# Performance work log

Measured on AMD Instinct MI355X. Metric: run time of the kernel, lower is better.

## Reference

```python
import jax, jax.numpy as jnp
import numpy as np
from jax import lax

BS, K, N = 8, 8, 16            # batch, gathers per sample, picks per curve
T, WG = 3072, 64               # gather time samples, traces
H, WC = 256, 256               # CVEncoder ScaleSize
RH, RW = 1024, 512             # resize (also GatherEncoder outLen=RH)
T0, T1 = 0.0, 7000.0           # tInt[0], tInt[-1]


def setup_inputs() -> dict:
    key = jax.random.key(0)
    ks = jax.random.split(key, 8)
    gather = jax.random.normal(ks[0], (BS, K, T, WG), jnp.float32)
    # cv: times sorted, strictly > 0, within [T0, T1]; velocities within VMM range
    times = jnp.sort(jax.random.uniform(ks[1], (BS, K, N), minval=100.0, maxval=T1), axis=-1)
    vels = jnp.sort(jax.random.uniform(ks[2], (BS, K, N), minval=1500.0, maxval=4500.0), axis=-1)
    cv = jnp.stack([times, vels], axis=-1).astype(jnp.float32)
    VMM = jnp.tile(jnp.array([1500.0, 4500.0], jnp.float32), (BS, 1))
    def cw(k, shape):
        return (jax.random.normal(k, shape, jnp.float32) * 0.1)
    params = dict(
        w1=cw(ks[3], (1, 1, 3, 3)), b1=jnp.zeros((1,), jnp.float32), g1=jnp.ones((1,), jnp.float32), be1=jnp.zeros((1,), jnp.float32),
        w2=cw(ks[4], (2, 3, 3, 3)), b2=jnp.zeros((2,), jnp.float32), g2=jnp.ones((2,), jnp.float32), be2=jnp.zeros((2,), jnp.float32),
        w3=cw(ks[5], (1, 2, 3, 2)), b3=jnp.zeros((1,), jnp.float32), g3=jnp.ones((1,), jnp.float32), be3=jnp.zeros((1,), jnp.float32),
        wf=cw(ks[6], (1, 1, 3, 3)), bf=jnp.zeros((1,), jnp.float32), gf=jnp.ones((1,), jnp.float32), bef=jnp.zeros((1,), jnp.float32),
    )
    return {"gather": gather, "cv": cv, "VMM": VMM, **params}


def _conv(x, w, b, stride, pad):
    y = lax.conv_general_dilated(x, w, stride, pad, dimension_numbers=("NCHW", "OIHW", "NCHW"))
    return y + b[None, :, None, None]


def _bn(x, g, b, eps=1e-5):
    # training-mode BatchNorm2d: stats over (N, H, W)
    m = jnp.mean(x, (0, 2, 3), keepdims=True)
    v = jnp.var(x, (0, 2, 3), keepdims=True)
    return (x - m) / jnp.sqrt(v + eps) * g[None, :, None, None] + b[None, :, None, None]


def _lrelu(x):
    return jnp.where(x >= 0, x, 0.1 * x)


def _cbl(x, w, b, g, be, stride):
    return _lrelu(_bn(_conv(x, w, b, stride, "VALID"), g, be))


def _maxpool(x, k):
    p = k // 2
    return lax.reduce_window(x, -jnp.inf, lax.max, (1, 1, k, k), (1, 1, 1, 1),
                             ((0, 0), (0, 0), (p, p), (p, p)))


def _cv_mask(cv, VMM):
    # normalize times to fractional row index and velocities to fractional col index
    dt = (T1 - T0) / (H - 1)
    t_idx = (cv[..., 0] - T0) / dt                                        # (BS,K,N)
    dv = (VMM[:, 1] - VMM[:, 0]) / (WC - 1)                               # (BS,)
    v_idx = (cv[..., 1] - VMM[:, 0, None, None]) / dv[:, None, None]      # (BS,K,N)
    t_flat = t_idx.reshape(-1, N)
    v_flat = v_idx.reshape(-1, N)
    tq = jnp.arange(H, dtype=jnp.float32)
    # per-curve piecewise-linear interpolation of v over the time grid
    v_curve = jax.vmap(lambda xp, fp: jnp.interp(tq, xp, fp))(t_flat, v_flat)  # (M,H)
    v_int = jnp.clip(v_curve.astype(jnp.int32), 0, WC - 1)
    M = BS * K
    mask = jnp.full((M, H, WC), 0.01, jnp.float32)
    mask = mask.at[jnp.arange(M)[:, None], jnp.arange(H)[None, :], v_int].add(0.9)
    mask = mask.reshape(BS, K, H, WC)
    # bilinear resize, half-pixel centers == torch align_corners=False
    return jax.image.resize(mask, (BS, K, RH, RW), method="linear")


def _forward(gather, cv, VMM, w1, b1, g1, be1, w2, b2, g2, be2, w3, b3, g3, be3, wf, bf, gf, bef):
    cv_mask = lax.stop_gradient(_cv_mask(cv, VMM))          # CVEncoder runs under no_grad
    x = gather.reshape(-1, 1, T, WG)                        # (BS*K,1,T,WG)
    x = x / jnp.max(jnp.abs(x))                             # mode='mute': keep sign
    x = _cbl(x, w1, b1, g1, be1, (3, 2))                    # (M,1,1024,31)
    xcat = jnp.concatenate([x, _maxpool(x, 3), _maxpool(x, 5)], axis=1)
    x = _cbl(xcat, w2, b2, g2, be2, (3, 2))                 # (M,2,341,15)
    x = _cbl(x, w3, b3, g3, be3, (3, 2))                    # (M,1,113,7)
    x = jax.image.resize(x, (x.shape[0], 1, RH, 1), method="linear")
    genr = x.reshape(BS, K, RH, 1)
    mix = jnp.sum(genr * cv_mask, axis=1, keepdims=True)    # (BS,1,RH,RW)
    y = _conv(mix, wf, bf, (1, 1), ((1, 1), (1, 1)))
    return _lrelu(_bn(y, gf, bef))


def reference(gather, cv, VMM, w1, b1, g1, be1, w2, b2, g2, be2, w3, b3, g3, be3, wf, bf, gf, bef):
    return _forward(gather, cv, VMM, w1, b1, g1, be1, w2, b2, g2, be2, w3, b3, g3, be3, wf, bf, gf, bef)
```

## Files before the change

kernel.cpp:

```cpp
#include <hip/hip_runtime.h>
#include <math.h>

#define BSZ 8
#define KG  8
#define NP  16
#define MM  64
#define TT  3072
#define WGN 64
#define HH  256
#define WCN 256
#define RHN 1024
#define RWN 512

#define C1H 1024
#define C1W 31
#define C2H 341
#define C2W 15
#define C3H 113
#define C3W 7

#define N1 (MM*C1H*C1W)
#define N2 (MM*C2H*C2W)
#define N3 (MM*C3H*C3W)
#define NF (BSZ*RHN*RWN)

#define SL 8

#define OFF_VINT 768
#define OFF_Y1   (OFF_VINT + MM*HH*4)
#define OFF_Y2   (OFF_Y1  + N1*4)
#define OFF_Y3   (OFF_Y2  + 2*N2*4)
#define OFF_GENR (OFF_Y3  + N3*4)

__device__ __forceinline__ void blockAdd2(double s, double ss, double* o0, double* o1) {
    __shared__ double red[4][2];
    __syncthreads();
    int lane = threadIdx.x & 63, wid = threadIdx.x >> 6;
#pragma unroll
    for (int off = 32; off > 0; off >>= 1) {
        s  += __shfl_down(s,  off, 64);
        ss += __shfl_down(ss, off, 64);
    }
    if (lane == 0) { red[wid][0] = s; red[wid][1] = ss; }
    __syncthreads();
    if (threadIdx.x == 0) {
        double a = 0, b = 0;
        int nw = blockDim.x >> 6;
        for (int i = 0; i < nw; i++) { a += red[i][0]; b += red[i][1]; }
        int slot = blockIdx.x & (SL - 1);
        atomicAdd(&o0[slot], a); atomicAdd(&o1[slot], b);
    }
}

__device__ __forceinline__ float2 bn_ab(const double* __restrict__ sums, int c,
                                        const float* __restrict__ g,
                                        const float* __restrict__ be, double n) {
    double sum = 0, sumsq = 0;
#pragma unroll
    for (int j = 0; j < SL; j++) {
        sum   += sums[(2 * c) * SL + j];
        sumsq += sums[(2 * c + 1) * SL + j];
    }
    double mean = sum / n;
    double var  = sumsq / n - mean * mean;
    double a = (double)g[c] / sqrt(var + 1e-5);
    return make_float2((float)a, (float)((double)be[c] - mean * a));
}

__global__ void k_conv1(const float* __restrict__ g, const float* __restrict__ w1,
                        const float* __restrict__ b1,
                        float* __restrict__ y1, double* sums) {
    float w[9];
#pragma unroll
    for (int i = 0; i < 9; i++) w[i] = w1[i];
    float bb = b1[0];
    double s = 0, ss = 0;
    int stride = gridDim.x * blockDim.x;
    for (int idx = blockIdx.x * blockDim.x + threadIdx.x; idx < N1; idx += stride) {
        int ow = idx % C1W;
        int t2 = idx / C1W;
        int oh = t2 % C1H;
        int m  = t2 / C1H;
        const float* xp = g + (size_t)m * TT * WGN + (size_t)(oh * 3) * WGN + ow * 2;
        float acc = bb;
#pragma unroll
        for (int r = 0; r < 3; r++)
#pragma unroll
            for (int c = 0; c < 3; c++) acc += w[r * 3 + c] * xp[r * WGN + c];
        y1[idx] = acc;
        s += acc; ss += (double)acc * (double)acc;
    }
    blockAdd2(s, ss, &sums[0], &sums[SL]);
}

#define F2_OH 32
#define F2_NCH 11
#define F2_NRMAX (3*F2_OH + 4)
__global__ void k_fused2(const float* __restrict__ y1, const double* __restrict__ sums_r,
                         const float* __restrict__ g1, const float* __restrict__ be1,
                         const float* __restrict__ w2, const float* __restrict__ b2,
                         float* __restrict__ y2, double* sums) {
    __shared__ float sact[F2_NRMAX][32];
    __shared__ float sr3[F2_NRMAX][32];
    __shared__ float sr5[F2_NRMAX][32];
    float2 ab1 = bn_ab(sums_r, 0, g1, be1, (double)N1);
    int m   = blockIdx.x / F2_NCH;
    int ch  = blockIdx.x % F2_NCH;
    int oh0 = ch * F2_OH;
    int OHa = min(F2_OH, C2H - oh0);
    int NR  = 3 * OHa + 4;
    int gl0 = 3 * oh0 - 2;
    const float* yp = y1 + (size_t)m * C1H * C1W;
    for (int i = threadIdx.x; i < NR * C1W; i += blockDim.x) {
        int l = i / C1W, w = i % C1W;
        int gr = gl0 + l;
        float v = -INFINITY;
        if (gr >= 0 && gr < C1H) {
            v = ab1.x * yp[gr * C1W + w] + ab1.y;
            v = v >= 0.f ? v : 0.1f * v;
        }
        sact[l][w] = v;
    }
    __syncthreads();
    for (int i = threadIdx.x; i < NR * C1W; i += blockDim.x) {
        int l = i / C1W, w = i % C1W;
        int wl1 = max(w - 1, 0), wr1 = min(w + 1, C1W - 1);
        int wl2 = max(w - 2, 0), wr2 = min(w + 2, C1W - 1);
        float c  = sact[l][w];
        float m3 = fmaxf(fmaxf(sact[l][wl1], c), sact[l][wr1]);
        float m5 = fmaxf(fmaxf(m3, sact[l][wl2]), sact[l][wr2]);
        sr3[l][w] = m3;
        sr5[l][w] = m5;
    }
    __syncthreads();
    double s0 = 0, ss0 = 0, s1 = 0, ss1 = 0;
    for (int o = threadIdx.x; o < OHa * C2W; o += blockDim.x) {
        int lo = o / C2W, ow = o % C2W;
        float a0 = b2[0], acc1 = b2[1];
#pragma unroll
        for (int i = 0; i < 3; i++) {
            int l = 3 * lo + 2 + i;
#pragma unroll
            for (int j = 0; j < 3; j++) {
                int wc = 2 * ow + j;
                float v0 = sact[l][wc];
                float v1 = fmaxf(fmaxf(sr3[l - 1][wc], sr3[l][wc]), sr3[l + 1][wc]);
                float v2 = fmaxf(fmaxf(fmaxf(sr5[l - 2][wc], sr5[l - 1][wc]), sr5[l][wc]),
                                 fmaxf(sr5[l + 1][wc], sr5[l + 2][wc]));
                int ki = i * 3 + j;
                a0   += w2[ki] * v0 + w2[9 + ki] * v1 + w2[18 + ki] * v2;
                acc1 += w2[27 + ki] * v0 + w2[36 + ki] * v1 + w2[45 + ki] * v2;
            }
        }
        size_t ob = (size_t)m * (2 * C2H * C2W) + (size_t)(oh0 + lo) * C2W + ow;
        y2[ob] = a0;
        y2[ob + C2H * C2W] = acc1;
        s0 += a0; ss0 += (double)a0 * a0;
        s1 += acc1; ss1 += (double)acc1 * acc1;
    }
    blockAdd2(s0, ss0, &sums[2 * SL], &sums[3 * SL]);
    blockAdd2(s1, ss1, &sums[4 * SL], &sums[5 * SL]);
}

__global__ void k_conv3(const float* __restrict__ y2, const double* __restrict__ sums_r,
                        const float* __restrict__ g2, const float* __restrict__ be2,
                        const float* __restrict__ w3, const float* __restrict__ b3,
                        float* __restrict__ y3, double* sums) {
    float2 ab20 = bn_ab(sums_r + 2 * SL, 0, g2, be2, (double)N2);
    float2 ab21 = bn_ab(sums_r + 2 * SL, 1, g2, be2, (double)N2);
    double s = 0, ss = 0;
    int stride = gridDim.x * blockDim.x;
    for (int idx = blockIdx.x * blockDim.x + threadIdx.x; idx < N3; idx += stride) {
        int ow = idx % C3W;
        int t2 = idx / C3W;
        int oh = t2 % C3H;
        int m  = t2 / C3H;
        float acc = b3[0];
#pragma unroll
        for (int i = 0; i < 2; i++) {
            float aa = i ? ab21.x : ab20.x, bb = i ? ab21.y : ab20.y;
            const float* cp = y2 + (size_t)m * (2 * C2H * C2W) + (size_t)i * C2H * C2W
                              + (size_t)(oh * 3) * C2W + ow * 2;
#pragma unroll
            for (int r = 0; r < 3; r++)
#pragma unroll
                for (int c = 0; c < 2; c++) {
                    float v = aa * cp[r * C2W + c] + bb;
                    v = v >= 0.f ? v : 0.1f * v;
                    acc += w3[i * 6 + r * 2 + c] * v;
                }
        }
        y3[idx] = acc;
        s += acc; ss += (double)acc * acc;
    }
    blockAdd2(s, ss, &sums[6 * SL], &sums[7 * SL]);
}

__global__ void k_vintgenr(const float* __restrict__ cv, const float* __restrict__ VMM,
                           const float* __restrict__ y3, const double* __restrict__ sums_r,
                           const float* __restrict__ g3, const float* __restrict__ be3,
                           int* __restrict__ vint, float* __restrict__ genr) {
    __shared__ float tt[NP], vv[NP];
    __shared__ float tile[C3H * C3W];
    int m = blockIdx.x;
    int b = m >> 3;
    float2 ab3 = bn_ab(sums_r + 6 * SL, 0, g3, be3, (double)N3);
    if (threadIdx.x < NP) {
        int n = threadIdx.x;
        float t = cv[(m * NP + n) * 2 + 0];
        float v = cv[(m * NP + n) * 2 + 1];
        float dt = 7000.0f / 255.0f;
        tt[n] = t / dt;
        float vmin = VMM[b * 2], vmax = VMM[b * 2 + 1];
        float dv = (vmax - vmin) / 255.0f;
        vv[n] = (v - vmin) / dv;
    }
    for (int i = threadIdx.x; i < C3H * C3W; i += blockDim.x) {
        float v = ab3.x * y3[m * C3H * C3W + i] + ab3.y;
        tile[i] = v >= 0.f ? v : 0.1f * v;
    }
    __syncthreads();
    {
        int h = threadIdx.x;
        float x = (float)h;
        float val;
        if (x <= tt[0]) val = vv[0];
        else if (x >= tt[NP - 1]) val = vv[NP - 1];
        else {
            int i = 1;
            while (i < NP - 1 && tt[i] <= x) i++;
            float d = tt[i] - tt[i - 1];
            val = (d != 0.f) ? vv[i - 1] + (x - tt[i - 1]) / d * (vv[i] - vv[i - 1]) : vv[i];
        }
        int vi = (int)val;
        vint[m * HH + h] = max(0, min(WCN - 1, vi));
    }
    const float cw0 = 4.f / 37.f, cw1 = 5.f / 37.f, cw2 = 6.f / 37.f, cw3 = 7.f / 37.f;
    const float cw[7] = { cw0, cw1, cw2, cw3, cw2, cw1, cw0 };
    for (int i = threadIdx.x; i < RHN; i += blockDim.x) {
        float sh = (i + 0.5f) * (113.0f / 1024.0f) - 0.5f;
        float fl = floorf(sh);
        float fr = sh - fl;
        int i0 = (int)fl, i1 = i0 + 1;
        i0 = max(0, min(C3H - 1, i0));
        i1 = max(0, min(C3H - 1, i1));
        float acc = 0.f;
#pragma unroll
        for (int x = 0; x < 7; x++) {
            float v = (1.f - fr) * tile[i0 * C3W + x] + fr * tile[i1 * C3W + x];
            acc += cw[x] * v;
        }
        genr[m * RHN + i] = acc;
    }
}

#define MC_TH 16
__device__ __forceinline__ void build_mix_tile(const float* __restrict__ genr,
                                               const int* __restrict__ vint,
                                               int b, int h0,
                                               float (*tile)[RWN + 2], float* Grow) {
    for (int i = threadIdx.x; i < (MC_TH + 2) * (RWN + 2); i += blockDim.x)
        ((float*)tile)[i] = 0.f;
    if (threadIdx.x < MC_TH + 2) Grow[threadIdx.x] = 0.f;
    __syncthreads();
    if (threadIdx.x < (MC_TH + 2) * KG) {
        int r = threadIdx.x / KG, k = threadIdx.x % KG;
        int h = h0 - 1 + r;
        if (h >= 0 && h < RHN) {
            int m = b * KG + k;
            float g = genr[m * RHN + h];
            atomicAdd(&Grow[r], g);
            float sh = (h + 0.5f) * 0.25f - 0.5f;
            float fl = floorf(sh);
            float fh = sh - fl;
            int ih0 = (int)fl, ih1 = ih0 + 1;
            ih0 = max(0, min(HH - 1, ih0));
            ih1 = max(0, min(HH - 1, ih1));
            int vv[2] = { vint[m * HH + ih0], vint[m * HH + ih1] };
            float aa[2] = { 0.9f * g * (1.f - fh), 0.9f * g * fh };
#pragma unroll
            for (int t = 0; t < 2; t++) {
                int v = vv[t]; float A = aa[t];
                if (v == 0) {
                    atomicAdd(&tile[r][1 + 0], A);
                    atomicAdd(&tile[r][1 + 1], 0.75f * A);
                    atomicAdd(&tile[r][1 + 2], 0.25f * A);
                } else if (v == WCN - 1) {
                    atomicAdd(&tile[r][1 + 509], 0.25f * A);
                    atomicAdd(&tile[r][1 + 510], 0.75f * A);
                    atomicAdd(&tile[r][1 + 511], A);
                } else {
                    atomicAdd(&tile[r][1 + 2 * v - 1], 0.25f * A);
                    atomicAdd(&tile[r][1 + 2 * v],     0.75f * A);
                    atomicAdd(&tile[r][1 + 2 * v + 1], 0.75f * A);
                    atomicAdd(&tile[r][1 + 2 * v + 2], 0.25f * A);
                }
            }
        }
    }
    __syncthreads();
    for (int i = threadIdx.x; i < (MC_TH + 2) * RWN; i += blockDim.x) {
        int r = i / RWN, w = i % RWN;
        int h = h0 - 1 + r;
        if (h >= 0 && h < RHN) tile[r][w + 1] += 0.01f * Grow[r];
    }
    __syncthreads();
}

__global__ void k_mixA(const float* __restrict__ genr, const int* __restrict__ vint,
                       const float* __restrict__ wf, const float* __restrict__ bf,
                       double* sums) {
    __shared__ float tile[MC_TH + 2][RWN + 2];
    __shared__ float Grow[MC_TH + 2];
    int b   = blockIdx.x / (RHN / MC_TH);
    int h0  = (blockIdx.x % (RHN / MC_TH)) * MC_TH;
    build_mix_tile(genr, vint, b, h0, tile, Grow);
    float w[9];
#pragma unroll
    for (int i = 0; i < 9; i++) w[i] = wf[i];
    float bb = bf[0];
    double s = 0, ss = 0;
    for (int o = threadIdx.x; o < MC_TH * RWN; o += blockDim.x) {
        int lr = o / RWN, x = o % RWN;
        float acc = bb;
#pragma unroll
        for (int dr = 0; dr < 3; dr++)
#pragma unroll
            for (int dc = 0; dc < 3; dc++)
                acc += w[dr * 3 + dc] * tile[lr + dr][x + dc];
        s += acc; ss += (double)acc * acc;
    }
    blockAdd2(s, ss, &sums[8 * SL], &sums[9 * SL]);
}

__global__ void k_mixB(const float* __restrict__ genr, const int* __restrict__ vint,
                       const float* __restrict__ wf, const float* __restrict__ bf,
                       const double* __restrict__ sums_r, const float* __restrict__ gf,
                       const float* __restrict__ bef, float* __restrict__ out) {
    __shared__ float tile[MC_TH + 2][RWN + 2];
    __shared__ float Grow[MC_TH + 2];
    float2 abf = bn_ab(sums_r + 8 * SL, 0, gf, bef, (double)NF);
    int b   = blockIdx.x / (RHN / MC_TH);
    int h0  = (blockIdx.x % (RHN / MC_TH)) * MC_TH;
    build_mix_tile(genr, vint, b, h0, tile, Grow);
    float w[9];
#pragma unroll
    for (int i = 0; i < 9; i++) w[i] = wf[i];
    float bb = bf[0];
    for (int o = threadIdx.x; o < MC_TH * RWN; o += blockDim.x) {
        int lr = o / RWN, x = o % RWN;
        float acc = bb;
#pragma unroll
        for (int dr = 0; dr < 3; dr++)
#pragma unroll
            for (int dc = 0; dc < 3; dc++)
                acc += w[dr * 3 + dc] * tile[lr + dr][x + dc];
        float v = abf.x * acc + abf.y;
        out[((size_t)b * RHN + (h0 + lr)) * RWN + x] = v >= 0.f ? v : 0.1f * v;
    }
}

extern "C" void kernel_launch(void* const* d_in, const int* in_sizes, int n_in,
                              void* d_out, int out_size, void* d_ws, size_t ws_size,
                              hipStream_t stream) {
    const float* gather = (const float*)d_in[0];
    const float* cv     = (const float*)d_in[1];
    const float* VMM    = (const float*)d_in[2];
    const float* w1 = (const float*)d_in[3];
    const float* b1 = (const float*)d_in[4];
    const float* g1 = (const float*)d_in[5];
    const float* be1 = (const float*)d_in[6];
    const float* w2 = (const float*)d_in[7];
    const float* b2 = (const float*)d_in[8];
    const float* g2 = (const float*)d_in[9];
    const float* be2 = (const float*)d_in[10];
    const float* w3 = (const float*)d_in[11];
    const float* b3 = (const float*)d_in[12];
    const float* g3 = (const float*)d_in[13];
    const float* be3 = (const float*)d_in[14];
    const float* wf = (const float*)d_in[15];
    const float* bf = (const float*)d_in[16];
    const float* gf = (const float*)d_in[17];
    const float* bef = (const float*)d_in[18];
    float* out = (float*)d_out;

    char* ws = (char*)d_ws;
    double* sums = (double*)ws;
    int*   vint  = (int*)(ws + OFF_VINT);
    float* y1    = (float*)(ws + OFF_Y1);
    float* y2    = (float*)(ws + OFF_Y2);
    float* y3    = (float*)(ws + OFF_Y3);
    float* genr  = (float*)(ws + OFF_GENR);

    hipMemsetAsync(d_ws, 0, 640, stream);

    k_conv1<<<512, 256, 0, stream>>>(gather, w1, b1, y1, sums);
    k_fused2<<<MM * F2_NCH, 256, 0, stream>>>(y1, sums, g1, be1, w2, b2, y2, sums);
    k_conv3<<<198, 256, 0, stream>>>(y2, sums, g2, be2, w3, b3, y3, sums);
    k_vintgenr<<<MM, 256, 0, stream>>>(cv, VMM, y3, sums, g3, be3, vint, genr);
    k_mixA<<<BSZ * (RHN / MC_TH), 256, 0, stream>>>(genr, vint, wf, bf, sums);
    k_mixB<<<BSZ * (RHN / MC_TH), 256, 0, stream>>>(genr, vint, wf, bf, sums, gf, bef, out);
}
```

Before: 196.9 us.

## Fuse all stages into one cooperative persistent kernel with grid syncs

Replaces six separate kernel launches with a single cooperative kernel of 512 blocks that uses grid.sync between the BatchNorm-dependent stages. The final mix conv keeps its 32 outputs per thread in registers, so the tile is built and convolved once instead of being rebuilt in a second pass just to apply BN. Conv1 now stages gather tiles in shared memory with float4 loads. This removes launch gaps and the duplicated mix work, at the cost of grid-wide barriers, a fixed grid size and register pressure from the accumulator array.

```diff
diff --git a/kernel.cpp b/kernel.cpp
--- a/kernel.cpp
+++ b/kernel.cpp
@@ -1,5 +1,8 @@
 #include <hip/hip_runtime.h>
+#include <hip/hip_cooperative_groups.h>
 #include <math.h>
+
+namespace cg = cooperative_groups;
 
 #define BSZ 8
 #define KG  8
@@ -25,6 +28,8 @@
 #define NF (BSZ*RHN*RWN)
 
 #define SL 8
+#define GRID 512
+#define BLK  256
 
 #define OFF_VINT 768
 #define OFF_Y1   (OFF_VINT + MM*HH*4)
@@ -32,7 +37,11 @@
 #define OFF_Y3   (OFF_Y2  + 2*N2*4)
 #define OFF_GENR (OFF_Y3  + N3*4)
 
-__device__ __forceinline__ void blockAdd2(double s, double ss, double* o0, double* o1) {
+#define MC_TH 16
+#define SMEM_BYTES 38400
+
+__device__ __forceinline__ void blockAdd2(double s, double ss, double* o0, double* o1,
+                                          int slot) {
     __shared__ double red[4][2];
     __syncthreads();
     int lane = threadIdx.x & 63, wid = threadIdx.x >> 6;
@@ -45,9 +54,8 @@
     __syncthreads();
     if (threadIdx.x == 0) {
         double a = 0, b = 0;
-        int nw = blockDim.x >> 6;
-        for (int i = 0; i < nw; i++) { a += red[i][0]; b += red[i][1]; }
-        int slot = blockIdx.x & (SL - 1);
+#pragma unroll
+        for (int i = 0; i < 4; i++) { a += red[i][0]; b += red[i][1]; }
         atomicAdd(&o0[slot], a); atomicAdd(&o1[slot], b);
     }
 }
@@ -67,296 +75,304 @@
     return make_float2((float)a, (float)((double)be[c] - mean * a));
 }
 
-__global__ void k_conv1(const float* __restrict__ g, const float* __restrict__ w1,
-                        const float* __restrict__ b1,
-                        float* __restrict__ y1, double* sums) {
-    float w[9];
-#pragma unroll
-    for (int i = 0; i < 9; i++) w[i] = w1[i];
-    float bb = b1[0];
-    double s = 0, ss = 0;
-    int stride = gridDim.x * blockDim.x;
-    for (int idx = blockIdx.x * blockDim.x + threadIdx.x; idx < N1; idx += stride) {
-        int ow = idx % C1W;
-        int t2 = idx / C1W;
-        int oh = t2 % C1H;
-        int m  = t2 / C1H;
-        const float* xp = g + (size_t)m * TT * WGN + (size_t)(oh * 3) * WGN + ow * 2;
-        float acc = bb;
-#pragma unroll
-        for (int r = 0; r < 3; r++)
-#pragma unroll
-            for (int c = 0; c < 3; c++) acc += w[r * 3 + c] * xp[r * WGN + c];
-        y1[idx] = acc;
-        s += acc; ss += (double)acc * (double)acc;
-    }
-    blockAdd2(s, ss, &sums[0], &sums[SL]);
-}
-
 #define F2_OH 32
 #define F2_NCH 11
-#define F2_NRMAX (3*F2_OH + 4)
-__global__ void k_fused2(const float* __restrict__ y1, const double* __restrict__ sums_r,
-                         const float* __restrict__ g1, const float* __restrict__ be1,
-                         const float* __restrict__ w2, const float* __restrict__ b2,
-                         float* __restrict__ y2, double* sums) {
-    __shared__ float sact[F2_NRMAX][32];
-    __shared__ float sr3[F2_NRMAX][32];
-    __shared__ float sr5[F2_NRMAX][32];
-    float2 ab1 = bn_ab(sums_r, 0, g1, be1, (double)N1);
-    int m   = blockIdx.x / F2_NCH;
-    int ch  = blockIdx.x % F2_NCH;
-    int oh0 = ch * F2_OH;
-    int OHa = min(F2_OH, C2H - oh0);
-    int NR  = 3 * OHa + 4;
-    int gl0 = 3 * oh0 - 2;
-    const float* yp = y1 + (size_t)m * C1H * C1W;
-    for (int i = threadIdx.x; i < NR * C1W; i += blockDim.x) {
-        int l = i / C1W, w = i % C1W;
-        int gr = gl0 + l;
-        float v = -INFINITY;
-        if (gr >= 0 && gr < C1H) {
-            v = ab1.x * yp[gr * C1W + w] + ab1.y;
-            v = v >= 0.f ? v : 0.1f * v;
-        }
-        sact[l][w] = v;
-    }
-    __syncthreads();
-    for (int i = threadIdx.x; i < NR * C1W; i += blockDim.x) {
-        int l = i / C1W, w = i % C1W;
-        int wl1 = max(w - 1, 0), wr1 = min(w + 1, C1W - 1);
-        int wl2 = max(w - 2, 0), wr2 = min(w + 2, C1W - 1);
-        float c  = sact[l][w];
-        float m3 = fmaxf(fmaxf(sact[l][wl1], c), sact[l][wr1]);
-        float m5 = fmaxf(fmaxf(m3, sact[l][wl2]), sact[l][wr2]);
-        sr3[l][w] = m3;
-        sr5[l][w] = m5;
-    }
-    __syncthreads();
-    double s0 = 0, ss0 = 0, s1 = 0, ss1 = 0;
-    for (int o = threadIdx.x; o < OHa * C2W; o += blockDim.x) {
-        int lo = o / C2W, ow = o % C2W;
-        float a0 = b2[0], acc1 = b2[1];
-#pragma unroll
-        for (int i = 0; i < 3; i++) {
-            int l = 3 * lo + 2 + i;
-#pragma unroll
-            for (int j = 0; j < 3; j++) {
-                int wc = 2 * ow + j;
-                float v0 = sact[l][wc];
-                float v1 = fmaxf(fmaxf(sr3[l - 1][wc], sr3[l][wc]), sr3[l + 1][wc]);
-                float v2 = fmaxf(fmaxf(fmaxf(sr5[l - 2][wc], sr5[l - 1][wc]), sr5[l][wc]),
-                                 fmaxf(sr5[l + 1][wc], sr5[l + 2][wc]));
-                int ki = i * 3 + j;
-                a0   += w2[ki] * v0 + w2[9 + ki] * v1 + w2[18 + ki] * v2;
-                acc1 += w2[27 + ki] * v0 + w2[36 + ki] * v1 + w2[45 + ki] * v2;
-            }
-        }
-        size_t ob = (size_t)m * (2 * C2H * C2W) + (size_t)(oh0 + lo) * C2W + ow;
-        y2[ob] = a0;
-        y2[ob + C2H * C2W] = acc1;
-        s0 += a0; ss0 += (double)a0 * a0;
-        s1 += acc1; ss1 += (double)acc1 * acc1;
-    }
-    blockAdd2(s0, ss0, &sums[2 * SL], &sums[3 * SL]);
-    blockAdd2(s1, ss1, &sums[4 * SL], &sums[5 * SL]);
-}
-
-__global__ void k_conv3(const float* __restrict__ y2, const double* __restrict__ sums_r,
-                        const float* __restrict__ g2, const float* __restrict__ be2,
-                        const float* __restrict__ w3, const float* __restrict__ b3,
-                        float* __restrict__ y3, double* sums) {
-    float2 ab20 = bn_ab(sums_r + 2 * SL, 0, g2, be2, (double)N2);
-    float2 ab21 = bn_ab(sums_r + 2 * SL, 1, g2, be2, (double)N2);
-    double s = 0, ss = 0;
-    int stride = gridDim.x * blockDim.x;
-    for (int idx = blockIdx.x * blockDim.x + threadIdx.x; idx < N3; idx += stride) {
-        int ow = idx % C3W;
-        int t2 = idx / C3W;
-        int oh = t2 % C3H;
-        int m  = t2 / C3H;
-        float acc = b3[0];
-#pragma unroll
-        for (int i = 0; i < 2; i++) {
-            float aa = i ? ab21.x : ab20.x, bb = i ? ab21.y : ab20.y;
-            const float* cp = y2 + (size_t)m * (2 * C2H * C2W) + (size_t)i * C2H * C2W
-                              + (size_t)(oh * 3) * C2W + ow * 2;
-#pragma unroll
-            for (int r = 0; r < 3; r++)
-#pragma unroll
-                for (int c = 0; c < 2; c++) {
-                    float v = aa * cp[r * C2W + c] + bb;
+
+__global__ void __launch_bounds__(BLK, 2) k_mega(
+        const float* __restrict__ gather, const float* __restrict__ cv,
+        const float* __restrict__ VMM,
+        const float* __restrict__ w1, const float* __restrict__ b1,
+        const float* __restrict__ g1, const float* __restrict__ be1,
+        const float* __restrict__ w2, const float* __restrict__ b2,
+        const float* __restrict__ g2, const float* __restrict__ be2,
+        const float* __restrict__ w3, const float* __restrict__ b3,
+        const float* __restrict__ g3, const float* __restrict__ be3,
+        const float* __restrict__ wf, const float* __restrict__ bf,
+        const float* __restrict__ gf, const float* __restrict__ bef,
+        double* sums, int* vint, float* y1, float* y2, float* y3, float* genr,
+        float* out) {
+    cg::grid_group grid = cg::this_grid();
+    __shared__ __align__(16) char smem[SMEM_BYTES];
+    int slot = blockIdx.x & (SL - 1);
+
+    {
+        float (*S1)[WGN] = (float (*)[WGN])smem;
+        float w[9];
+#pragma unroll
+        for (int i = 0; i < 9; i++) w[i] = w1[i];
+        float bb = b1[0];
+        double s = 0, ss = 0;
+        for (int tile = blockIdx.x; tile < MM * 32; tile += GRID) {
+            int m = tile >> 5, t32 = tile & 31;
+            int oh0 = t32 * F2_OH;
+            const float4* g4 = (const float4*)(gather + (size_t)m * TT * WGN
+                                               + (size_t)(3 * oh0) * WGN);
+            float4* s4 = (float4*)smem;
+            __syncthreads();
+#pragma unroll
+            for (int i = threadIdx.x; i < 96 * WGN / 4; i += BLK) s4[i] = g4[i];
+            __syncthreads();
+#pragma unroll
+            for (int j = 0; j < 4; j++) {
+                int o = threadIdx.x + j * BLK;
+                if (o < F2_OH * C1W) {
+                    int lo = o / C1W, ow = o % C1W;
+                    float acc = bb;
+#pragma unroll
+                    for (int r = 0; r < 3; r++)
+#pragma unroll
+                        for (int c = 0; c < 3; c++)
+                            acc += w[r * 3 + c] * S1[3 * lo + r][2 * ow + c];
+                    y1[(size_t)m * C1H * C1W + (size_t)(oh0 + lo) * C1W + ow] = acc;
+                    s += acc; ss += (double)acc * acc;
+                }
+            }
+        }
+        blockAdd2(s, ss, &sums[0], &sums[SL], slot);
+    }
+    __threadfence(); grid.sync();
+
+    {
+        float (*sact)[32] = (float (*)[32])smem;
+        float (*sr3)[32]  = (float (*)[32])(smem + 12800);
+        float (*sr5)[32]  = (float (*)[32])(smem + 25600);
+        float2 ab1 = bn_ab(sums, 0, g1, be1, (double)N1);
+        double s0 = 0, ss0 = 0, s1 = 0, ss1 = 0;
+        for (int vb = blockIdx.x; vb < MM * F2_NCH; vb += GRID) {
+            int m   = vb / F2_NCH;
+            int ch  = vb % F2_NCH;
+            int oh0 = ch * F2_OH;
+            int OHa = min(F2_OH, C2H - oh0);
+            int NR  = 3 * OHa + 4;
+            int gl0 = 3 * oh0 - 2;
+            const float* yp = y1 + (size_t)m * C1H * C1W;
+            __syncthreads();
+            for (int i = threadIdx.x; i < NR * C1W; i += BLK) {
+                int l = i / C1W, w = i % C1W;
+                int gr = gl0 + l;
+                float v = -INFINITY;
+                if (gr >= 0 && gr < C1H) {
+                    v = ab1.x * yp[gr * C1W + w] + ab1.y;
                     v = v >= 0.f ? v : 0.1f * v;
-                    acc += w3[i * 6 + r * 2 + c] * v;
                 }
-        }
-        y3[idx] = acc;
-        s += acc; ss += (double)acc * acc;
-    }
-    blockAdd2(s, ss, &sums[6 * SL], &sums[7 * SL]);
-}
-
-__global__ void k_vintgenr(const float* __restrict__ cv, const float* __restrict__ VMM,
-                           const float* __restrict__ y3, const double* __restrict__ sums_r,
-                           const float* __restrict__ g3, const float* __restrict__ be3,
-                           int* __restrict__ vint, float* __restrict__ genr) {
-    __shared__ float tt[NP], vv[NP];
-    __shared__ float tile[C3H * C3W];
-    int m = blockIdx.x;
-    int b = m >> 3;
-    float2 ab3 = bn_ab(sums_r + 6 * SL, 0, g3, be3, (double)N3);
-    if (threadIdx.x < NP) {
-        int n = threadIdx.x;
-        float t = cv[(m * NP + n) * 2 + 0];
-        float v = cv[(m * NP + n) * 2 + 1];
-        float dt = 7000.0f / 255.0f;
-        tt[n] = t / dt;
-        float vmin = VMM[b * 2], vmax = VMM[b * 2 + 1];
-        float dv = (vmax - vmin) / 255.0f;
-        vv[n] = (v - vmin) / dv;
-    }
-    for (int i = threadIdx.x; i < C3H * C3W; i += blockDim.x) {
-        float v = ab3.x * y3[m * C3H * C3W + i] + ab3.y;
-        tile[i] = v >= 0.f ? v : 0.1f * v;
-    }
-    __syncthreads();
+                sact[l][w] = v;
+            }
+            __syncthreads();
+            for (int i = threadIdx.x; i < NR * C1W; i += BLK) {
+                int l = i / C1W, w = i % C1W;
+                int wl1 = max(w - 1, 0), wr1 = min(w + 1, C1W - 1);
+                int wl2 = max(w - 2, 0), wr2 = min(w + 2, C1W - 1);
+                float c  = sact[l][w];
+                float m3 = fmaxf(fmaxf(sact[l][wl1], c), sact[l][wr1]);
+                float m5 = fmaxf(fmaxf(m3, sact[l][wl2]), sact[l][wr2]);
+                sr3[l][w] = m3;
+                sr5[l][w] = m5;
+            }
+            __syncthreads();
+            for (int o = threadIdx.x; o < OHa * C2W; o += BLK) {
+                int lo = o / C2W, ow = o % C2W;
+                float a0 = b2[0], acc1 = b2[1];
+#pragma unroll
+                for (int i = 0; i < 3; i++) {
+                    int l = 3 * lo + 2 + i;
+#pragma unroll
+                    for (int j = 0; j < 3; j++) {
+                        int wc = 2 * ow + j;
+                        float v0 = sact[l][wc];
+                        float v1 = fmaxf(fmaxf(sr3[l - 1][wc], sr3[l][wc]), sr3[l + 1][wc]);
+                        float v2 = fmaxf(fmaxf(fmaxf(sr5[l - 2][wc], sr5[l - 1][wc]),
+                                               sr5[l][wc]),
+                                         fmaxf(sr5[l + 1][wc], sr5[l + 2][wc]));
+                        int ki = i * 3 + j;
+                        a0   += w2[ki] * v0 + w2[9 + ki] * v1 + w2[18 + ki] * v2;
+                        acc1 += w2[27 + ki] * v0 + w2[36 + ki] * v1 + w2[45 + ki] * v2;
+                    }
+                }
+                size_t ob = (size_t)m * (2 * C2H * C2W) + (size_t)(oh0 + lo) * C2W + ow;
+                y2[ob] = a0;
+                y2[ob + C2H * C2W] = acc1;
+                s0 += a0; ss0 += (double)a0 * a0;
+                s1 += acc1; ss1 += (double)acc1 * acc1;
+            }
+        }
+        blockAdd2(s0, ss0, &sums[2 * SL], &sums[3 * SL], slot);
+        blockAdd2(s1, ss1, &sums[4 * SL], &sums[5 * SL], slot);
+    }
+    __threadfence(); grid.sync();
+
     {
-        int h = threadIdx.x;
-        float x = (float)h;
-        float val;
-        if (x <= tt[0]) val = vv[0];
-        else if (x >= tt[NP - 1]) val = vv[NP - 1];
-        else {
-            int i = 1;
-            while (i < NP - 1 && tt[i] <= x) i++;
-            float d = tt[i] - tt[i - 1];
-            val = (d != 0.f) ? vv[i - 1] + (x - tt[i - 1]) / d * (vv[i] - vv[i - 1]) : vv[i];
-        }
-        int vi = (int)val;
-        vint[m * HH + h] = max(0, min(WCN - 1, vi));
-    }
-    const float cw0 = 4.f / 37.f, cw1 = 5.f / 37.f, cw2 = 6.f / 37.f, cw3 = 7.f / 37.f;
-    const float cw[7] = { cw0, cw1, cw2, cw3, cw2, cw1, cw0 };
-    for (int i = threadIdx.x; i < RHN; i += blockDim.x) {
-        float sh = (i + 0.5f) * (113.0f / 1024.0f) - 0.5f;
-        float fl = floorf(sh);
-        float fr = sh - fl;
-        int i0 = (int)fl, i1 = i0 + 1;
-        i0 = max(0, min(C3H - 1, i0));
-        i1 = max(0, min(C3H - 1, i1));
-        float acc = 0.f;
-#pragma unroll
-        for (int x = 0; x < 7; x++) {
-            float v = (1.f - fr) * tile[i0 * C3W + x] + fr * tile[i1 * C3W + x];
-            acc += cw[x] * v;
-        }
-        genr[m * RHN + i] = acc;
-    }
-}
-
-#define MC_TH 16
-__device__ __forceinline__ void build_mix_tile(const float* __restrict__ genr,
-                                               const int* __restrict__ vint,
-                                               int b, int h0,
-                                               float (*tile)[RWN + 2], float* Grow) {
-    for (int i = threadIdx.x; i < (MC_TH + 2) * (RWN + 2); i += blockDim.x)
-        ((float*)tile)[i] = 0.f;
-    if (threadIdx.x < MC_TH + 2) Grow[threadIdx.x] = 0.f;
-    __syncthreads();
-    if (threadIdx.x < (MC_TH + 2) * KG) {
-        int r = threadIdx.x / KG, k = threadIdx.x % KG;
-        int h = h0 - 1 + r;
-        if (h >= 0 && h < RHN) {
-            int m = b * KG + k;
-            float g = genr[m * RHN + h];
-            atomicAdd(&Grow[r], g);
-            float sh = (h + 0.5f) * 0.25f - 0.5f;
+        float2 ab20 = bn_ab(sums + 2 * SL, 0, g2, be2, (double)N2);
+        float2 ab21 = bn_ab(sums + 2 * SL, 1, g2, be2, (double)N2);
+        double s = 0, ss = 0;
+        for (int idx = blockIdx.x * BLK + threadIdx.x; idx < N3; idx += GRID * BLK) {
+            int ow = idx % C3W;
+            int t2 = idx / C3W;
+            int oh = t2 % C3H;
+            int m  = t2 / C3H;
+            float acc = b3[0];
+#pragma unroll
+            for (int i = 0; i < 2; i++) {
+                float aa = i ? ab21.x : ab20.x, bb = i ? ab21.y : ab20.y;
+                const float* cp = y2 + (size_t)m * (2 * C2H * C2W) + (size_t)i * C2H * C2W
+                                  + (size_t)(oh * 3) * C2W + ow * 2;
+#pragma unroll
+                for (int r = 0; r < 3; r++)
+#pragma unroll
+                    for (int c = 0; c < 2; c++) {
+                        float v = aa * cp[r * C2W + c] + bb;
+                        v = v >= 0.f ? v : 0.1f * v;
+                        acc += w3[i * 6 + r * 2 + c] * v;
+                    }
+            }
+            y3[idx] = acc;
+            s += acc; ss += (double)acc * acc;
+        }
+        blockAdd2(s, ss, &sums[6 * SL], &sums[7 * SL], slot);
+    }
+    __threadfence(); grid.sync();
+
+    if (blockIdx.x < MM) {
+        float* tts  = (float*)smem;
+        float* vvs  = tts + NP;
+        float* tile = vvs + NP;
+        int m = blockIdx.x;
+        int b = m >> 3;
+        float2 ab3 = bn_ab(sums + 6 * SL, 0, g3, be3, (double)N3);
+        __syncthreads();
+        if (threadIdx.x < NP) {
+            int n = threadIdx.x;
+            float t = cv[(m * NP + n) * 2 + 0];
+            float v = cv[(m * NP + n) * 2 + 1];
+            float dt = 7000.0f / 255.0f;
+            tts[n] = t / dt;
+            float vmin = VMM[b * 2], vmax = VMM[b * 2 + 1];
+            float dv = (vmax - vmin) / 255.0f;
+            vvs[n] = (v - vmin) / dv;
+        }
+        for (int i = threadIdx.x; i < C3H * C3W; i += BLK) {
+            float v = ab3.x * y3[m * C3H * C3W + i] + ab3.y;
+            tile[i] = v >= 0.f ? v : 0.1f * v;
+        }
+        __syncthreads();
+        {
+            int h = threadIdx.x;
+            float x = (float)h;
+            float val;
+            if (x <= tts[0]) val = vvs[0];
+            else if (x >= tts[NP - 1]) val = vvs[NP - 1];
+            else {
+                int i = 1;
+                while (i < NP - 1 && tts[i] <= x) i++;
+                float d = tts[i] - tts[i - 1];
+                val = (d != 0.f) ? vvs[i - 1] + (x - tts[i - 1]) / d * (vvs[i] - vvs[i - 1])
+                                 : vvs[i];
+            }
+            int vi = (int)val;
+            vint[m * HH + h] = max(0, min(WCN - 1, vi));
+        }
+        const float cwv[7] = { 4.f/37.f, 5.f/37.f, 6.f/37.f, 7.f/37.f,
+                               6.f/37.f, 5.f/37.f, 4.f/37.f };
+        for (int i = threadIdx.x; i < RHN; i += BLK) {
+            float sh = (i + 0.5f) * (113.0f / 1024.0f) - 0.5f;
             float fl = floorf(sh);
-            float fh = sh - fl;
-            int ih0 = (int)fl, ih1 = ih0 + 1;
-            ih0 = max(0, min(HH - 1, ih0));
-            ih1 = max(0, min(HH - 1, ih1));
-            int vv[2] = { vint[m * HH + ih0], vint[m * HH + ih1] };
-            float aa[2] = { 0.9f * g * (1.f - fh), 0.9f * g * fh };
-#pragma unroll
-            for (int t = 0; t < 2; t++) {
-                int v = vv[t]; float A = aa[t];
-                if (v == 0) {
-                    atomicAdd(&tile[r][1 + 0], A);
-                    atomicAdd(&tile[r][1 + 1], 0.75f * A);
-                    atomicAdd(&tile[r][1 + 2], 0.25f * A);
-                } else if (v == WCN - 1) {
-                    atomicAdd(&tile[r][1 + 509], 0.25f * A);
-                    atomicAdd(&tile[r][1 + 510], 0.75f * A);
-                    atomicAdd(&tile[r][1 + 511], A);
-                } else {
-                    atomicAdd(&tile[r][1 + 2 * v - 1], 0.25f * A);
-                    atomicAdd(&tile[r][1 + 2 * v],     0.75f * A);
-                    atomicAdd(&tile[r][1 + 2 * v + 1], 0.75f * A);
-                    atomicAdd(&tile[r][1 + 2 * v + 2], 0.25f * A);
+            float fr = sh - fl;
+            int i0 = (int)fl, i1 = i0 + 1;
+            i0 = max(0, min(C3H - 1, i0));
+            i1 = max(0, min(C3H - 1, i1));
+            float acc = 0.f;
+#pragma unroll
+            for (int x = 0; x < 7; x++) {
+                float v = (1.f - fr) * tile[i0 * C3W + x] + fr * tile[i1 * C3W + x];
+                acc += cwv[x] * v;
+            }
+            genr[m * RHN + i] = acc;
+        }
+    }
+    __threadfence(); grid.sync();
+
+    float accv[32];
+    int b5  = blockIdx.x >> 6;
+    int h0  = (blockIdx.x & 63) * MC_TH;
+    {
+        float (*tile)[RWN + 2] = (float (*)[RWN + 2])smem;
+        float* Grow = (float*)(smem + (MC_TH + 2) * (RWN + 2) * 4);
+        for (int i = threadIdx.x; i < (MC_TH + 2) * (RWN + 2); i += BLK)
+            ((float*)tile)[i] = 0.f;
+        if (threadIdx.x < MC_TH + 2) Grow[threadIdx.x] = 0.f;
+        __syncthreads();
+        if (threadIdx.x < (MC_TH + 2) * KG) {
+            int r = threadIdx.x / KG, k = threadIdx.x % KG;
+            int h = h0 - 1 + r;
+            if (h >= 0 && h < RHN) {
+                int m = b5 * KG + k;
+                float g = genr[m * RHN + h];
+                atomicAdd(&Grow[r], g);
+                float sh = (h + 0.5f) * 0.25f - 0.5f;
+                float fl = floorf(sh);
+                float fh = sh - fl;
+                int ih0 = (int)fl, ih1 = ih0 + 1;
+                ih0 = max(0, min(HH - 1, ih0));
+                ih1 = max(0, min(HH - 1, ih1));
+                int vv2[2] = { vint[m * HH + ih0], vint[m * HH + ih1] };
+                float aa2[2] = { 0.9f * g * (1.f - fh), 0.9f * g * fh };
+#pragma unroll
+                for (int t = 0; t < 2; t++) {
+                    int v = vv2[t]; float A = aa2[t];
+                    if (v == 0) {
+                        atomicAdd(&tile[r][1 + 0], A);
+                        atomicAdd(&tile[r][1 + 1], 0.75f * A);
+                        atomicAdd(&tile[r][1 + 2], 0.25f * A);
+                    } else if (v == WCN - 1) {
+                        atomicAdd(&tile[r][1 + 509], 0.25f * A);
+                        atomicAdd(&tile[r][1 + 510], 0.75f * A);
+                        atomicAdd(&tile[r][1 + 511], A);
+                    } else {
+                        atomicAdd(&tile[r][1 + 2 * v - 1], 0.25f * A);
+                        atomicAdd(&tile[r][1 + 2 * v],     0.75f * A);
+                        atomicAdd(&tile[r][1 + 2 * v + 1], 0.75f * A);
+                        atomicAdd(&tile[r][1 + 2 * v + 2], 0.25f * A);
+                    }
                 }
             }
         }
-    }
-    __syncthreads();
-    for (int i = threadIdx.x; i < (MC_TH + 2) * RWN; i += blockDim.x) {
-        int r = i / RWN, w = i % RWN;
-        int h = h0 - 1 + r;
-        if (h >= 0 && h < RHN) tile[r][w + 1] += 0.01f * Grow[r];
-    }
-    __syncthreads();
-}
-
-__global__ void k_mixA(const float* __restrict__ genr, const int* __restrict__ vint,
-                       const float* __restrict__ wf, const float* __restrict__ bf,
-                       double* sums) {
-    __shared__ float tile[MC_TH + 2][RWN + 2];
-    __shared__ float Grow[MC_TH + 2];
-    int b   = blockIdx.x / (RHN / MC_TH);
-    int h0  = (blockIdx.x % (RHN / MC_TH)) * MC_TH;
-    build_mix_tile(genr, vint, b, h0, tile, Grow);
-    float w[9];
-#pragma unroll
-    for (int i = 0; i < 9; i++) w[i] = wf[i];
-    float bb = bf[0];
-    double s = 0, ss = 0;
-    for (int o = threadIdx.x; o < MC_TH * RWN; o += blockDim.x) {
-        int lr = o / RWN, x = o % RWN;
-        float acc = bb;
-#pragma unroll
-        for (int dr = 0; dr < 3; dr++)
-#pragma unroll
-            for (int dc = 0; dc < 3; dc++)
-                acc += w[dr * 3 + dc] * tile[lr + dr][x + dc];
-        s += acc; ss += (double)acc * acc;
-    }
-    blockAdd2(s, ss, &sums[8 * SL], &sums[9 * SL]);
-}
-
-__global__ void k_mixB(const float* __restrict__ genr, const int* __restrict__ vint,
-                       const float* __restrict__ wf, const float* __restrict__ bf,
-                       const double* __restrict__ sums_r, const float* __restrict__ gf,
-                       const float* __restrict__ bef, float* __restrict__ out) {
-    __shared__ float tile[MC_TH + 2][RWN + 2];
-    __shared__ float Grow[MC_TH + 2];
-    float2 abf = bn_ab(sums_r + 8 * SL, 0, gf, bef, (double)NF);
-    int b   = blockIdx.x / (RHN / MC_TH);
-    int h0  = (blockIdx.x % (RHN / MC_TH)) * MC_TH;
-    build_mix_tile(genr, vint, b, h0, tile, Grow);
-    float w[9];
-#pragma unroll
-    for (int i = 0; i < 9; i++) w[i] = wf[i];
-    float bb = bf[0];
-    for (int o = threadIdx.x; o < MC_TH * RWN; o += blockDim.x) {
-        int lr = o / RWN, x = o % RWN;
-        float acc = bb;
-#pragma unroll
-        for (int dr = 0; dr < 3; dr++)
-#pragma unroll
-            for (int dc = 0; dc < 3; dc++)
-                acc += w[dr * 3 + dc] * tile[lr + dr][x + dc];
-        float v = abf.x * acc + abf.y;
-        out[((size_t)b * RHN + (h0 + lr)) * RWN + x] = v >= 0.f ? v : 0.1f * v;
+        __syncthreads();
+        for (int i = threadIdx.x; i < (MC_TH + 2) * RWN; i += BLK) {
+            int r = i / RWN, w = i % RWN;
+            int h = h0 - 1 + r;
+            if (h >= 0 && h < RHN) tile[r][w + 1] += 0.01f * Grow[r];
+        }
+        __syncthreads();
+        float w[9];
+#pragma unroll
+        for (int i = 0; i < 9; i++) w[i] = wf[i];
+        float bb = bf[0];
+        double s = 0, ss = 0;
+#pragma unroll
+        for (int j = 0; j < 32; j++) {
+            int o  = threadIdx.x + j * BLK;
+            int lr = o >> 9, x = o & 511;
+            float acc = bb;
+#pragma unroll
+            for (int dr = 0; dr < 3; dr++)
+#pragma unroll
+                for (int dc = 0; dc < 3; dc++)
+                    acc += w[dr * 3 + dc] * tile[lr + dr][x + dc];
+            accv[j] = acc;
+            s += acc; ss += (double)acc * acc;
+        }
+        blockAdd2(s, ss, &sums[8 * SL], &sums[9 * SL], slot);
+    }
+    __threadfence(); grid.sync();
+
+    {
+        float2 abf = bn_ab(sums + 8 * SL, 0, gf, bef, (double)NF);
+#pragma unroll
+        for (int j = 0; j < 32; j++) {
+            int o  = threadIdx.x + j * BLK;
+            int lr = o >> 9, x = o & 511;
+            float v = abf.x * accv[j] + abf.y;
+            out[((size_t)b5 * RHN + (h0 + lr)) * RWN + x] = v >= 0.f ? v : 0.1f * v;
+        }
     }
 }
 
@@ -394,10 +410,12 @@
 
     hipMemsetAsync(d_ws, 0, 640, stream);
 
-    k_conv1<<<512, 256, 0, stream>>>(gather, w1, b1, y1, sums);
-    k_fused2<<<MM * F2_NCH, 256, 0, stream>>>(y1, sums, g1, be1, w2, b2, y2, sums);
-    k_conv3<<<198, 256, 0, stream>>>(y2, sums, g2, be2, w3, b3, y3, sums);
-    k_vintgenr<<<MM, 256, 0, stream>>>(cv, VMM, y3, sums, g3, be3, vint, genr);
-    k_mixA<<<BSZ * (RHN / MC_TH), 256, 0, stream>>>(genr, vint, wf, bf, sums);
-    k_mixB<<<BSZ * (RHN / MC_TH), 256, 0, stream>>>(genr, vint, wf, bf, sums, gf, bef, out);
+    void* args[] = { (void*)&gather, (void*)&cv, (void*)&VMM,
+                     (void*)&w1, (void*)&b1, (void*)&g1, (void*)&be1,
+                     (void*)&w2, (void*)&b2, (void*)&g2, (void*)&be2,
+                     (void*)&w3, (void*)&b3, (void*)&g3, (void*)&be3,
+                     (void*)&wf, (void*)&bf, (void*)&gf, (void*)&bef,
+                     (void*)&sums, (void*)&vint, (void*)&y1, (void*)&y2,
+                     (void*)&y3, (void*)&genr, (void*)&out };
+    hipLaunchCooperativeKernel((void*)k_mega, dim3(GRID), dim3(BLK), args, 0, stream);
 }
```

Measured after the change: 645.7 us. 228% more time.
